# Kernel tuning notes

Measured on AMD Instinct MI355X. Metric: run time of the kernel, lower is better.

## Reference

```python
import jax, jax.numpy as jnp
import numpy as np
from jax import lax


def setup_inputs() -> dict:
    key = jax.random.key(0)
    k1, k2 = jax.random.split(key)
    L, B, D = 1024, 16, 1024
    x = jax.random.normal(k1, (L, B, D), dtype=jnp.float32)
    # weight maps n_in -> n_out*k with k=3 (n_in == n_out); small scale for stability
    weight = jax.random.normal(k2, (D, 3 * D), dtype=jnp.float32) * 0.05
    bias = jnp.zeros((2 * D,), dtype=jnp.float32)
    c0 = jnp.zeros((B, D), dtype=jnp.float32)
    return {"x": x, "weight": weight, "bias": bias, "c0": c0}


def reference(x, weight, bias, c0):
    # SRUCell forward, k == 3 (n_in == n_out), unidirectional, tanh activation,
    # no dropout masks (mask_h == NULL -> mask = 1).
    L, B, D = x.shape
    u = (x.reshape(L * B, D) @ weight).reshape(L, B, D, 3)
    b1 = bias[:D]
    b2 = bias[D:]
    u0 = u[..., 0]                                   # [L, B, D]
    g1 = jax.nn.sigmoid(u[..., 1] + b1)              # forget gate
    g2 = jax.nn.sigmoid(u[..., 2] + b2)              # reset/highway gate

    def step(c, inp):
        u0_t, g1_t, g2_t, x_t = inp
        c_new = (c - u0_t) * g1_t + u0_t             # c = c'*g1 + u0*(1-g1)
        h_t = (jnp.tanh(c_new) - x_t) * g2_t + x_t   # h = act(c)*g2 + x*(1-g2)
        return c_new, h_t

    c_last, h = lax.scan(step, c0, (u0, g1, g2, x))
    return h, c_last
```

## Files before the change

kernel.cpp:

```cpp
#include <hip/hip_runtime.h>

#define L_DIM 1024
#define B_DIM 16
#define D_DIM 1024
#define K_DIM 1024
#define N_DIM 3072
#define M_DIM (L_DIM * B_DIM)
#define CHAINS 16384
#define CHUNK 32
#define NCHUNK 32

typedef float f32x4 __attribute__((ext_vector_type(4)));
typedef __bf16 bf16x8 __attribute__((ext_vector_type(8)));
typedef unsigned short u16;
typedef unsigned int u32;

__device__ __forceinline__ u16 f2bf(float f) {
  u32 u = __float_as_uint(f);
  u = u + 0x7FFFu + ((u >> 16) & 1u);
  return (u16)(u >> 16);
}
__device__ __forceinline__ float bf2f(u16 v) {
  return __uint_as_float(((u32)v) << 16);
}
__device__ __forceinline__ float bf2f_lo(u32 v) {
  return __uint_as_float(v << 16);
}
__device__ __forceinline__ float bf2f_hi(u32 v) {
  return __uint_as_float(v & 0xffff0000u);
}
__device__ __forceinline__ float fexp(float v) {
  return __builtin_amdgcn_exp2f(v * 1.4426950408889634f);
}
__device__ __forceinline__ float sigm(float z) {
  return __builtin_amdgcn_rcpf(1.0f + fexp(-z));
}
__device__ __forceinline__ float ftanh(float v) {
  return 1.0f - 2.0f * __builtin_amdgcn_rcpf(1.0f + fexp(2.0f * v));
}

__global__ __launch_bounds__(256) void cvt_x_kernel(const float4* __restrict__ in,
                                                    ushort4* __restrict__ out, int n4) {
  int i = blockIdx.x * 256 + threadIdx.x;
  if (i < n4) {
    float4 v = in[i];
    ushort4 o;
    o.x = f2bf(v.x); o.y = f2bf(v.y); o.z = f2bf(v.z); o.w = f2bf(v.w);
    out[i] = o;
  }
}

__global__ __launch_bounds__(256) void cvt_w_kernel(const float* __restrict__ W,
                                                    u16* __restrict__ Wt) {
  __shared__ float tile[64][65];
  int c0 = blockIdx.x * 64;
  int r0 = blockIdx.y * 64;
  int tx = threadIdx.x & 63;
  int ty = threadIdx.x >> 6;
#pragma unroll
  for (int i = 0; i < 16; ++i) {
    int row = i * 4 + ty;
    tile[row][tx] = W[(size_t)(r0 + row) * N_DIM + c0 + tx];
  }
  __syncthreads();
#pragma unroll
  for (int i = 0; i < 16; ++i) {
    int crow = i * 4 + ty;
    int c = c0 + crow;
    int nprime = (c % 3) * D_DIM + (c / 3);
    Wt[(size_t)nprime * K_DIM + r0 + tx] = f2bf(tile[tx][crow]);
  }
}


#define AS1 __attribute__((address_space(1)))
#define AS3 __attribute__((address_space(3)))
#define STAGE(gp, lp) do { \
  __builtin_amdgcn_global_load_lds((const AS1 void*)(gp), (AS3 void*)(lp), 16, 0, 0); \
  __builtin_amdgcn_global_load_lds((const AS1 void*)((gp) + (size_t)64 * K_DIM), \
                                   (AS3 void*)((lp) + 4096), 16, 0, 0); \
} while (0)

#define QUAD(AI, JB, BF) \
  _Pragma("unroll") \
  for (int i = 0; i < 4; ++i) { \
    _Pragma("unroll") \
    for (int j = 0; j < 2; ++j) { \
      acc[AI + i][JB + j] = __builtin_amdgcn_mfma_f32_16x16x32_bf16(aF[i][0], BF[j][0], acc[AI + i][JB + j], 0, 0, 0); \
      acc[AI + i][JB + j] = __builtin_amdgcn_mfma_f32_16x16x32_bf16(aF[i][1], BF[j][1], acc[AI + i][JB + j], 0, 0, 0); \
    } \
  }

__global__ __launch_bounds__(512, 2) void gemm_kernel(const u16* __restrict__ A,
                                                      const u16* __restrict__ Bt,
                                                      u16* __restrict__ U) {
  __shared__ __align__(16) u16 sm[65536];
  const int tid = threadIdx.x;
  const int wave = tid >> 6;
  const int lane = tid & 63;
  const int wm = wave >> 2;
  const int wn = wave & 3;
  const int quad = lane >> 4;
  const int l16 = lane & 15;

  const int flat = blockIdx.y * 12 + blockIdx.x;
  const int swz = (flat & 7) * 96 + (flat >> 3);
  const int m0 = (swz / 12) * 256;
  const int n0 = (swz % 12) * 256;

  const int rr = tid >> 3;
  const int slot = (tid & 7) ^ (rr & 7);
  const u16* gA = A + (size_t)(m0 + rr) * K_DIM + slot * 8;
  const u16* gB = Bt + (size_t)(n0 + rr) * K_DIM + slot * 8;

  u16* ldsA = sm + wave * 512;
  u16* ldsB = sm + 32768 + wave * 512;

  const int swzu = (l16 & 7) << 3;
  const int c0 = (quad * 8) ^ swzu;
  const int c1 = (32 + quad * 8) ^ swzu;
  const u16* pA = sm + (wm * 128 + l16) * 64;
  const u16* pB = sm + 32768 + (wn * 64 + l16) * 64;

  f32x4 acc[8][4] = {};

  STAGE(gA, ldsA);
  STAGE(gA + (size_t)128 * K_DIM, ldsA + 8192);
  STAGE(gB, ldsB);
  STAGE(gB + (size_t)128 * K_DIM, ldsB + 8192);
  STAGE(gB + 64, ldsB + 16384);
  STAGE(gB + (size_t)128 * K_DIM + 64, ldsB + 16384 + 8192);
  asm volatile("s_waitcnt vmcnt(0)" ::: "memory");
  __builtin_amdgcn_s_barrier();

  for (int u = 0; u < 16; ++u) {
    const int buf = u & 1;
    const int nb = buf ^ 1;
    const u16* pAb = pA + buf * 16384;
    const u16* pBb = pB + buf * 16384;
    bf16x8 aF[4][2], bLo[2][2], bHi[2][2];

#pragma unroll
    for (int i = 0; i < 4; ++i) {
      aF[i][0] = *(const bf16x8*)(pAb + i * 1024 + c0);
      aF[i][1] = *(const bf16x8*)(pAb + i * 1024 + c1);
    }
#pragma unroll
    for (int j = 0; j < 2; ++j) {
      bLo[j][0] = *(const bf16x8*)(pBb + j * 1024 + c0);
      bLo[j][1] = *(const bf16x8*)(pBb + j * 1024 + c1);
    }
    if (u < 15) STAGE(gA + (u + 1) * 64, ldsA + nb * 16384);
    __builtin_amdgcn_s_barrier();
    __builtin_amdgcn_s_setprio(1);
    QUAD(0, 0, bLo)
    __builtin_amdgcn_s_setprio(0);
    __builtin_amdgcn_s_barrier();

#pragma unroll
    for (int j = 0; j < 2; ++j) {
      bHi[j][0] = *(const bf16x8*)(pBb + (2 + j) * 1024 + c0);
      bHi[j][1] = *(const bf16x8*)(pBb + (2 + j) * 1024 + c1);
    }
    if (u < 15) STAGE(gA + (size_t)128 * K_DIM + (u + 1) * 64, ldsA + nb * 16384 + 8192);
    __builtin_amdgcn_s_barrier();
    __builtin_amdgcn_s_setprio(1);
    QUAD(0, 2, bHi)
    __builtin_amdgcn_s_setprio(0);
    __builtin_amdgcn_s_barrier();

#pragma unroll
    for (int i = 0; i < 4; ++i) {
      aF[i][0] = *(const bf16x8*)(pAb + (4 + i) * 1024 + c0);
      aF[i][1] = *(const bf16x8*)(pAb + (4 + i) * 1024 + c1);
    }
    if (u < 14) STAGE(gB + (u + 2) * 64, ldsB + buf * 16384);
    __builtin_amdgcn_s_barrier();
    __builtin_amdgcn_s_setprio(1);
    QUAD(4, 2, bHi)
    __builtin_amdgcn_s_setprio(0);
    __builtin_amdgcn_s_barrier();

    if (u < 14) {
      STAGE(gB + (size_t)128 * K_DIM + (u + 2) * 64, ldsB + buf * 16384 + 8192);
      asm volatile("s_waitcnt vmcnt(4)" ::: "memory");
    } else if (u == 14) {
      asm volatile("s_waitcnt vmcnt(0)" ::: "memory");
    }
    __builtin_amdgcn_s_barrier();
    __builtin_amdgcn_s_setprio(1);
    QUAD(4, 0, bLo)
    __builtin_amdgcn_s_setprio(0);
    __builtin_amdgcn_s_barrier();
  }

#pragma unroll
  for (int i = 0; i < 8; ++i) {
#pragma unroll
    for (int j = 0; j < 4; ++j) {
      const int col = n0 + wn * 64 + j * 16 + l16;
      const int rb = m0 + wm * 128 + i * 16 + quad * 4;
#pragma unroll
      for (int r = 0; r < 4; ++r)
        U[(size_t)(rb + r) * N_DIM + col] = f2bf(acc[i][j][r]);
    }
  }
}


__global__ __launch_bounds__(512) void sru_fused(const u16* __restrict__ U,
                                                 const float* __restrict__ x,
                                                 const float* __restrict__ bias,
                                                 const float* __restrict__ c0,
                                                 float* __restrict__ h,
                                                 float* __restrict__ clast) {
  __shared__ float sA[NCHUNK][32];
  __shared__ float sB[NCHUNK][32];
  __shared__ float sC[NCHUNK][32];

  const int flat = blockIdx.x;
  const int cb = (flat & 7) * 64 + (flat >> 3);
  const int b  = cb >> 5;
  const int d0 = (cb & 31) << 5;
  const int t  = threadIdx.x;
  const int pr = t & 15;
  const int j  = t >> 4;
  const int d2 = d0 + pr * 2;

  const float2 bb1 = *(const float2*)(bias + d2);

  {
    const u16* p = U + (size_t)(j * CHUNK * B_DIM + b) * N_DIM + d2;
    float A0 = 1.0f, A1 = 1.0f, B0 = 0.0f, B1 = 0.0f;
#pragma unroll 4
    for (int s = 0; s < CHUNK; ++s) {
      u32 w0 = *(const u32*)p;
      u32 w1 = *(const u32*)(p + D_DIM);
      float u0a = bf2f_lo(w0), u0b = bf2f_hi(w0);
      float g1a = sigm(bf2f_lo(w1) + bb1.x);
      float g1b = sigm(bf2f_hi(w1) + bb1.y);
      B0 = (B0 - u0a) * g1a + u0a;
      B1 = (B1 - u0b) * g1b + u0b;
      A0 *= g1a;
      A1 *= g1b;
      p += (size_t)B_DIM * N_DIM;
    }
    *(float2*)&sA[j][pr * 2] = make_float2(A0, A1);
    *(float2*)&sB[j][pr * 2] = make_float2(B0, B1);
  }
  __syncthreads();

  if (t < 32) {
    const int chain = cb * 32 + t;
    float c = c0[chain];
#pragma unroll
    for (int jj = 0; jj < NCHUNK; ++jj) {
      sC[jj][t] = c;
      c = sA[jj][t] * c + sB[jj][t];
    }
    clast[chain] = c;
  }
  __syncthreads();

  {
    const float2 bb2 = *(const float2*)(bias + D_DIM + d2);
    float2 c = *(const float2*)&sC[j][pr * 2];
    const size_t m0 = (size_t)(j * CHUNK * B_DIM + b);
    const u16* p = U + m0 * N_DIM + d2;
    const float* xp = x + m0 * D_DIM + d2;
    float* hp = h + m0 * D_DIM + d2;
#pragma unroll 4
    for (int s = 0; s < CHUNK; ++s) {
      u32 w0 = *(const u32*)p;
      u32 w1 = *(const u32*)(p + D_DIM);
      u32 w2 = *(const u32*)(p + 2 * D_DIM);
      float2 xv = *(const float2*)xp;
      float u0a = bf2f_lo(w0), u0b = bf2f_hi(w0);
      float g1a = sigm(bf2f_lo(w1) + bb1.x);
      float g1b = sigm(bf2f_hi(w1) + bb1.y);
      float g2a = sigm(bf2f_lo(w2) + bb2.x);
      float g2b = sigm(bf2f_hi(w2) + bb2.y);
      c.x = (c.x - u0a) * g1a + u0a;
      c.y = (c.y - u0b) * g1b + u0b;
      float2 hv;
      hv.x = (ftanh(c.x) - xv.x) * g2a + xv.x;
      hv.y = (ftanh(c.y) - xv.y) * g2b + xv.y;
      *(float2*)hp = hv;
      p += (size_t)B_DIM * N_DIM;
      xp += B_DIM * D_DIM;
      hp += B_DIM * D_DIM;
    }
  }
}

extern "C" void kernel_launch(void* const* d_in, const int* in_sizes, int n_in,
                              void* d_out, int out_size, void* d_ws, size_t ws_size,
                              hipStream_t stream) {
  const float* x = (const float*)d_in[0];
  const float* W = (const float*)d_in[1];
  const float* bias = (const float*)d_in[2];
  const float* c0 = (const float*)d_in[3];
  float* out = (float*)d_out;

  char* ws = (char*)d_ws;
  u16* xb = (u16*)ws;
  u16* wt = (u16*)(ws + 33554432);
  u16* U = (u16*)(ws + 33554432 + 6291456);

  cvt_x_kernel<<<16384, 256, 0, stream>>>((const float4*)x, (ushort4*)xb, M_DIM * K_DIM / 4);
  cvt_w_kernel<<<dim3(48, 16), 256, 0, stream>>>(W, wt);
  gemm_kernel<<<dim3(N_DIM / 256, M_DIM / 256), 512, 0, stream>>>(xb, wt, U);
  sru_fused<<<512, 512, 0, stream>>>(U, x, bias, c0, out, out + (size_t)M_DIM * D_DIM);
}
```

Measured before the change: 285.9 us.

## Fuse conversion kernels, deepen GEMM A prefetch, widen SRU scan blocks

Merges the x and W bf16 conversion kernels into one launch with a block-index split, removing one kernel launch. The GEMM now prefetches A two k-steps ahead, like B, and issues loads in pairs with a relaxed vmcnt wait, so more loads stay in flight per iteration. The SRU scan kernel moves to 1024-thread blocks covering 64 channels each, halving the grid to 256 blocks. The risks are lower occupancy or fewer blocks than CUs in the scan kernel, and subtle buffer hazards in the rescheduled prefetch.

After: 280.2 us. -2.0%, faster.

```diff
diff --git a/kernel.cpp b/kernel.cpp
--- a/kernel.cpp
+++ b/kernel.cpp
@@ -39,36 +39,36 @@
   return 1.0f - 2.0f * __builtin_amdgcn_rcpf(1.0f + fexp(2.0f * v));
 }
 
-__global__ __launch_bounds__(256) void cvt_x_kernel(const float4* __restrict__ in,
-                                                    ushort4* __restrict__ out, int n4) {
-  int i = blockIdx.x * 256 + threadIdx.x;
-  if (i < n4) {
-    float4 v = in[i];
+__global__ __launch_bounds__(256) void cvt_fused(const float4* __restrict__ xin,
+                                                 ushort4* __restrict__ xout,
+                                                 const float* __restrict__ W,
+                                                 u16* __restrict__ Wt) {
+  if (blockIdx.x < 16384) {
+    int i = blockIdx.x * 256 + threadIdx.x;
+    float4 v = xin[i];
     ushort4 o;
     o.x = f2bf(v.x); o.y = f2bf(v.y); o.z = f2bf(v.z); o.w = f2bf(v.w);
-    out[i] = o;
-  }
-}
-
-__global__ __launch_bounds__(256) void cvt_w_kernel(const float* __restrict__ W,
-                                                    u16* __restrict__ Wt) {
-  __shared__ float tile[64][65];
-  int c0 = blockIdx.x * 64;
-  int r0 = blockIdx.y * 64;
-  int tx = threadIdx.x & 63;
-  int ty = threadIdx.x >> 6;
-#pragma unroll
-  for (int i = 0; i < 16; ++i) {
-    int row = i * 4 + ty;
-    tile[row][tx] = W[(size_t)(r0 + row) * N_DIM + c0 + tx];
-  }
-  __syncthreads();
-#pragma unroll
-  for (int i = 0; i < 16; ++i) {
-    int crow = i * 4 + ty;
-    int c = c0 + crow;
-    int nprime = (c % 3) * D_DIM + (c / 3);
-    Wt[(size_t)nprime * K_DIM + r0 + tx] = f2bf(tile[tx][crow]);
+    xout[i] = o;
+  } else {
+    __shared__ float tile[64][65];
+    int wb = blockIdx.x - 16384;
+    int c0 = (wb % 48) * 64;
+    int r0 = (wb / 48) * 64;
+    int tx = threadIdx.x & 63;
+    int ty = threadIdx.x >> 6;
+#pragma unroll
+    for (int i = 0; i < 16; ++i) {
+      int row = i * 4 + ty;
+      tile[row][tx] = W[(size_t)(r0 + row) * N_DIM + c0 + tx];
+    }
+    __syncthreads();
+#pragma unroll
+    for (int i = 0; i < 16; ++i) {
+      int crow = i * 4 + ty;
+      int c = c0 + crow;
+      int nprime = (c % 3) * D_DIM + (c / 3);
+      Wt[(size_t)nprime * K_DIM + r0 + tx] = f2bf(tile[tx][crow]);
+    }
   }
 }
 
@@ -128,14 +128,15 @@
   STAGE(gA + (size_t)128 * K_DIM, ldsA + 8192);
   STAGE(gB, ldsB);
   STAGE(gB + (size_t)128 * K_DIM, ldsB + 8192);
+  STAGE(gA + 64, ldsA + 16384);
+  STAGE(gA + (size_t)128 * K_DIM + 64, ldsA + 16384 + 8192);
   STAGE(gB + 64, ldsB + 16384);
   STAGE(gB + (size_t)128 * K_DIM + 64, ldsB + 16384 + 8192);
-  asm volatile("s_waitcnt vmcnt(0)" ::: "memory");
+  asm volatile("s_waitcnt vmcnt(8)" ::: "memory");
   __builtin_amdgcn_s_barrier();
 
   for (int u = 0; u < 16; ++u) {
     const int buf = u & 1;
-    const int nb = buf ^ 1;
     const u16* pAb = pA + buf * 16384;
     const u16* pBb = pB + buf * 16384;
     bf16x8 aF[4][2], bLo[2][2], bHi[2][2];
@@ -150,7 +151,6 @@
       bLo[j][0] = *(const bf16x8*)(pBb + j * 1024 + c0);
       bLo[j][1] = *(const bf16x8*)(pBb + j * 1024 + c1);
     }
-    if (u < 15) STAGE(gA + (u + 1) * 64, ldsA + nb * 16384);
     __builtin_amdgcn_s_barrier();
     __builtin_amdgcn_s_setprio(1);
     QUAD(0, 0, bLo)
@@ -162,7 +162,6 @@
       bHi[j][0] = *(const bf16x8*)(pBb + (2 + j) * 1024 + c0);
       bHi[j][1] = *(const bf16x8*)(pBb + (2 + j) * 1024 + c1);
     }
-    if (u < 15) STAGE(gA + (size_t)128 * K_DIM + (u + 1) * 64, ldsA + nb * 16384 + 8192);
     __builtin_amdgcn_s_barrier();
     __builtin_amdgcn_s_setprio(1);
     QUAD(0, 2, bHi)
@@ -174,7 +173,10 @@
       aF[i][0] = *(const bf16x8*)(pAb + (4 + i) * 1024 + c0);
       aF[i][1] = *(const bf16x8*)(pAb + (4 + i) * 1024 + c1);
     }
-    if (u < 14) STAGE(gB + (u + 2) * 64, ldsB + buf * 16384);
+    if (u < 14) {
+      STAGE(gB + (u + 2) * 64, ldsB + buf * 16384);
+      STAGE(gB + (size_t)128 * K_DIM + (u + 2) * 64, ldsB + buf * 16384 + 8192);
+    }
     __builtin_amdgcn_s_barrier();
     __builtin_amdgcn_s_setprio(1);
     QUAD(4, 2, bHi)
@@ -182,8 +184,9 @@
     __builtin_amdgcn_s_barrier();
 
     if (u < 14) {
-      STAGE(gB + (size_t)128 * K_DIM + (u + 2) * 64, ldsB + buf * 16384 + 8192);
-      asm volatile("s_waitcnt vmcnt(4)" ::: "memory");
+      STAGE(gA + (u + 2) * 64, ldsA + buf * 16384);
+      STAGE(gA + (size_t)128 * K_DIM + (u + 2) * 64, ldsA + buf * 16384 + 8192);
+      asm volatile("s_waitcnt vmcnt(8)" ::: "memory");
     } else if (u == 14) {
       asm volatile("s_waitcnt vmcnt(0)" ::: "memory");
     }
@@ -208,23 +211,23 @@
 }
 
 
-__global__ __launch_bounds__(512) void sru_fused(const u16* __restrict__ U,
-                                                 const float* __restrict__ x,
-                                                 const float* __restrict__ bias,
-                                                 const float* __restrict__ c0,
-                                                 float* __restrict__ h,
-                                                 float* __restrict__ clast) {
-  __shared__ float sA[NCHUNK][32];
-  __shared__ float sB[NCHUNK][32];
-  __shared__ float sC[NCHUNK][32];
+__global__ __launch_bounds__(1024) void sru_fused(const u16* __restrict__ U,
+                                                  const float* __restrict__ x,
+                                                  const float* __restrict__ bias,
+                                                  const float* __restrict__ c0,
+                                                  float* __restrict__ h,
+                                                  float* __restrict__ clast) {
+  __shared__ float sA[NCHUNK][64];
+  __shared__ float sB[NCHUNK][64];
+  __shared__ float sC[NCHUNK][64];
 
   const int flat = blockIdx.x;
-  const int cb = (flat & 7) * 64 + (flat >> 3);
-  const int b  = cb >> 5;
-  const int d0 = (cb & 31) << 5;
+  const int cb = (flat & 7) * 32 + (flat >> 3);
+  const int b  = cb >> 4;
+  const int d0 = (cb & 15) << 6;
   const int t  = threadIdx.x;
-  const int pr = t & 15;
-  const int j  = t >> 4;
+  const int pr = t & 31;
+  const int j  = t >> 5;
   const int d2 = d0 + pr * 2;
 
   const float2 bb1 = *(const float2*)(bias + d2);
@@ -250,8 +253,8 @@
   }
   __syncthreads();
 
-  if (t < 32) {
-    const int chain = cb * 32 + t;
+  if (t < 64) {
+    const int chain = cb * 64 + t;
     float c = c0[chain];
 #pragma unroll
     for (int jj = 0; jj < NCHUNK; ++jj) {
@@ -307,8 +310,7 @@
   u16* wt = (u16*)(ws + 33554432);
   u16* U = (u16*)(ws + 33554432 + 6291456);
 
-  cvt_x_kernel<<<16384, 256, 0, stream>>>((const float4*)x, (ushort4*)xb, M_DIM * K_DIM / 4);
-  cvt_w_kernel<<<dim3(48, 16), 256, 0, stream>>>(W, wt);
+  cvt_fused<<<16384 + 768, 256, 0, stream>>>((const float4*)x, (ushort4*)xb, W, wt);
   gemm_kernel<<<dim3(N_DIM / 256, M_DIM / 256), 512, 0, stream>>>(xb, wt, U);
-  sru_fused<<<512, 512, 0, stream>>>(U, x, bias, c0, out, out + (size_t)M_DIM * D_DIM);
-}
+  sru_fused<<<256, 1024, 0, stream>>>(U, x, bias, c0, out, out + (size_t)M_DIM * D_DIM);
+}
```
